# Performance work log

Measured on AMD Instinct MI355X. Metric: run time of the kernel, lower is better.

Reference implementation:

```python
import jax, jax.numpy as jnp
import numpy as np

BZ, NF, D = 8, 10000, 16
H = W = 512


def setup_inputs() -> dict:
    key = jax.random.key(0)
    k1, k2, k3 = jax.random.split(key, 3)
    attrs = jax.random.normal(k1, (BZ, NF, 3, D), dtype=jnp.float32)
    # barycentric weights: positive, sum to 1 over the 3 vertices
    u = jax.random.uniform(k2, (BZ, H, W, 3), dtype=jnp.float32, minval=1e-3, maxval=1.0)
    baryw_buffer = u / jnp.sum(u, axis=-1, keepdims=True)
    # triangle indices into the flattened [BZ*NF] face table; -1 = empty pixel
    triangle_buffer = jax.random.randint(k3, (BZ, H, W), -1, BZ * NF, dtype=jnp.int32)
    return {"attrs": attrs, "baryw_buffer": baryw_buffer, "triangle_buffer": triangle_buffer}


def reference(attrs, baryw_buffer, triangle_buffer):
    # attrs: [N, NF, 3, D]; baryw_buffer: [N, H, W, 3]; triangle_buffer: [N, H, W] int (-1 = bg)
    N, H_, W_ = triangle_buffer.shape
    Dd = attrs.shape[-1]
    flat_attrs = attrs.reshape(-1, 3, Dd)                      # [N*NF, 3, D]
    mask = triangle_buffer == -1                               # [N, H, W]
    idx = jnp.where(mask, 0, triangle_buffer)                  # clamp bg to 0
    pixel_face_vals = flat_attrs[idx]                          # [N, H, W, 3, D] gather
    pixel_vals = jnp.einsum('nhwk,nhwkd->nhwd', baryw_buffer, pixel_face_vals)
    pixel_vals = jnp.where(mask[..., None], 0.0, pixel_vals)   # zero background
    out = jnp.moveaxis(pixel_vals, -1, 1)                      # [N, D, H, W]
    vis = (~mask).astype(jnp.float32)[:, None]                 # [N, 1, H, W]
    return jnp.concatenate([out, vis], axis=1)                 # [N, D+1, H, W]
```

## Files before the change

### kernel.cpp

```cpp
#include <hip/hip_runtime.h>
#include <hip/hip_fp16.h>

constexpr int BZ = 8, NF = 10000, D = 16, HImg = 512, WImg = 512;
constexpr int HW = HImg * WImg;
constexpr int NPIX = BZ * HW;
constexpr int NFACES = BZ * NF;
constexpr int PIX_PER_THREAD = 4;
constexpr int NTHREADS = NPIX / PIX_PER_THREAD;
constexpr int BLOCK = 256;
constexpr size_t REC_USHORTS = 64;
constexpr size_t WS_NEEDED = (size_t)NFACES * 128;

__global__ __launch_bounds__(BLOCK) void convert_kernel(
    const float* __restrict__ attrs, ushort* __restrict__ rec)
{
    const int tid = blockIdx.x * BLOCK + threadIdx.x;
    if (tid >= NFACES * 6) return;
    const int face = tid / 6;
    const int c    = tid - face * 6;
    const float4* src = reinterpret_cast<const float4*>(
        attrs + (size_t)face * 48 + c * 8);
    const float4 a = src[0], b = src[1];
    __half h[8];
    h[0] = __float2half_rn(a.x); h[1] = __float2half_rn(a.y);
    h[2] = __float2half_rn(a.z); h[3] = __float2half_rn(a.w);
    h[4] = __float2half_rn(b.x); h[5] = __float2half_rn(b.y);
    h[6] = __float2half_rn(b.z); h[7] = __float2half_rn(b.w);
    *reinterpret_cast<int4*>(rec + (size_t)face * REC_USHORTS + c * 8) =
        *reinterpret_cast<const int4*>(h);
}

__device__ inline void h8_to_f8(int4 raw, float f[8]) {
    const __half2* hp = reinterpret_cast<const __half2*>(&raw);
#pragma unroll
    for (int q = 0; q < 4; ++q) {
        const float2 t = __half22float2(hp[q]);
        f[2 * q]     = t.x;
        f[2 * q + 1] = t.y;
    }
}

__global__ __launch_bounds__(BLOCK) void render_f16_kernel(
    const ushort* __restrict__ rec,
    const float*  __restrict__ baryw,
    const int*    __restrict__ tri,
    float*        __restrict__ out)
{
    const int tid = blockIdx.x * BLOCK + threadIdx.x;
    const int p0  = tid * PIX_PER_THREAD;
    if (p0 >= NPIX) return;

    const int n   = p0 / HW;
    const int pix = p0 - n * HW;

    const int4 t4 = *reinterpret_cast<const int4*>(tri + p0);
    const float4* bw = reinterpret_cast<const float4*>(baryw + (size_t)p0 * 3);
    const float4 b0 = bw[0], b1 = bw[1], b2 = bw[2];

    float w[PIX_PER_THREAD][3] = {
        {b0.x, b0.y, b0.z},
        {b0.w, b1.x, b1.y},
        {b1.z, b1.w, b2.x},
        {b2.y, b2.z, b2.w},
    };
    const int t[PIX_PER_THREAD] = {t4.x, t4.y, t4.z, t4.w};

    float vis[PIX_PER_THREAD];
    const int4* rbase[PIX_PER_THREAD];
#pragma unroll
    for (int j = 0; j < PIX_PER_THREAD; ++j) {
        const bool bg = (t[j] < 0);
        vis[j] = bg ? 0.0f : 1.0f;
        const int tc = bg ? 0 : t[j];
        rbase[j] = reinterpret_cast<const int4*>(rec) + (size_t)tc * 8;
        w[j][0] *= vis[j];
        w[j][1] *= vis[j];
        w[j][2] *= vis[j];
    }

    const size_t outbase = (size_t)n * (D + 1) * HW + pix;

#pragma unroll
    for (int c = 0; c < 2; ++c) {
        float r[PIX_PER_THREAD][8];
#pragma unroll
        for (int j = 0; j < PIX_PER_THREAD; ++j) {
            const int4 A0 = rbase[j][0 + c];
            const int4 A1 = rbase[j][2 + c];
            const int4 A2 = rbase[j][4 + c];
            float a0[8], a1[8], a2[8];
            h8_to_f8(A0, a0);
            h8_to_f8(A1, a1);
            h8_to_f8(A2, a2);
#pragma unroll
            for (int i = 0; i < 8; ++i)
                r[j][i] = w[j][0] * a0[i] + w[j][1] * a1[i] + w[j][2] * a2[i];
        }
#pragma unroll
        for (int i = 0; i < 8; ++i) {
            const int d = c * 8 + i;
            float4 o;
            o.x = r[0][i]; o.y = r[1][i]; o.z = r[2][i]; o.w = r[3][i];
            *reinterpret_cast<float4*>(out + outbase + (size_t)d * HW) = o;
        }
    }

    float4 v;
    v.x = vis[0]; v.y = vis[1]; v.z = vis[2]; v.w = vis[3];
    *reinterpret_cast<float4*>(out + outbase + (size_t)D * HW) = v;
}

__global__ __launch_bounds__(BLOCK) void renderer_f32_kernel(
    const float* __restrict__ attrs,
    const float* __restrict__ baryw,
    const int*   __restrict__ tri,
    float*       __restrict__ out)
{
    const int tid = blockIdx.x * BLOCK + threadIdx.x;
    const int p0  = tid * PIX_PER_THREAD;
    if (p0 >= NPIX) return;

    const int n   = p0 / HW;
    const int pix = p0 - n * HW;

    const int4 t4 = *reinterpret_cast<const int4*>(tri + p0);
    const float4* bw = reinterpret_cast<const float4*>(baryw + (size_t)p0 * 3);
    const float4 b0 = bw[0], b1 = bw[1], b2 = bw[2];

    float w[PIX_PER_THREAD][3] = {
        {b0.x, b0.y, b0.z},
        {b0.w, b1.x, b1.y},
        {b1.z, b1.w, b2.x},
        {b2.y, b2.z, b2.w},
    };
    const int t[PIX_PER_THREAD] = {t4.x, t4.y, t4.z, t4.w};

    float vis[PIX_PER_THREAD];
    const float4* abase[PIX_PER_THREAD];
#pragma unroll
    for (int j = 0; j < PIX_PER_THREAD; ++j) {
        const bool bg = (t[j] < 0);
        vis[j] = bg ? 0.0f : 1.0f;
        const int tc = bg ? 0 : t[j];
        abase[j] = reinterpret_cast<const float4*>(attrs + (size_t)tc * (3 * D));
        w[j][0] *= vis[j];
        w[j][1] *= vis[j];
        w[j][2] *= vis[j];
    }

    const size_t outbase = (size_t)n * (D + 1) * HW + pix;

#pragma unroll
    for (int c = 0; c < 4; ++c) {
        float r[PIX_PER_THREAD][4];
#pragma unroll
        for (int j = 0; j < PIX_PER_THREAD; ++j) {
            const float4 a0 = abase[j][c];
            const float4 a1 = abase[j][4 + c];
            const float4 a2 = abase[j][8 + c];
            r[j][0] = w[j][0] * a0.x + w[j][1] * a1.x + w[j][2] * a2.x;
            r[j][1] = w[j][0] * a0.y + w[j][1] * a1.y + w[j][2] * a2.y;
            r[j][2] = w[j][0] * a0.z + w[j][1] * a1.z + w[j][2] * a2.z;
            r[j][3] = w[j][0] * a0.w + w[j][1] * a1.w + w[j][2] * a2.w;
        }
#pragma unroll
        for (int i = 0; i < 4; ++i) {
            const int d = c * 4 + i;
            float4 o;
            o.x = r[0][i]; o.y = r[1][i]; o.z = r[2][i]; o.w = r[3][i];
            *reinterpret_cast<float4*>(out + outbase + (size_t)d * HW) = o;
        }
    }

    float4 v;
    v.x = vis[0]; v.y = vis[1]; v.z = vis[2]; v.w = vis[3];
    *reinterpret_cast<float4*>(out + outbase + (size_t)D * HW) = v;
}

extern "C" void kernel_launch(void* const* d_in, const int* in_sizes, int n_in,
                              void* d_out, int out_size, void* d_ws, size_t ws_size,
                              hipStream_t stream) {
    const float* attrs = (const float*)d_in[0];
    const float* baryw = (const float*)d_in[1];
    const int*   tri   = (const int*)d_in[2];
    float*       out   = (float*)d_out;

    const int grid = NTHREADS / BLOCK;

    if (ws_size >= WS_NEEDED) {
        ushort* rec = (ushort*)d_ws;
        const int conv_grid = (NFACES * 6 + BLOCK - 1) / BLOCK;
        convert_kernel<<<conv_grid, BLOCK, 0, stream>>>(attrs, rec);
        render_f16_kernel<<<grid, BLOCK, 0, stream>>>(rec, baryw, tri, out);
    } else {
        renderer_f32_kernel<<<grid, BLOCK, 0, stream>>>(attrs, baryw, tri, out);
    }
}
```

Before: 230.6 us.

## Phase face-record gathers by index range with block barriers and nontemporal streaming

The f16 render kernel now splits the face table into four index ranges and gathers, inside each range, only the pixels whose triangle falls there. Block-level barriers between phases try to keep the gather working set small enough to stay cache-resident. Streaming inputs and outputs use nontemporal loads and stores so they do not evict the face records. The cost is extra barriers and divergent, predicated gathers. Block-level syncs do not align phases across the whole GPU, so the locality benefit is uncertain.

```diff
diff --git a/kernel.cpp b/kernel.cpp
--- a/kernel.cpp
+++ b/kernel.cpp
@@ -10,6 +10,12 @@
 constexpr int BLOCK = 256;
 constexpr size_t REC_USHORTS = 64;
 constexpr size_t WS_NEEDED = (size_t)NFACES * 128;
+
+constexpr int NPHASE = 4;
+constexpr int FACES_PER_PHASE = NFACES / NPHASE;
+
+typedef float f32x4 __attribute__((ext_vector_type(4)));
+typedef int   i32x4 __attribute__((ext_vector_type(4)));
 
 __global__ __launch_bounds__(BLOCK) void convert_kernel(
     const float* __restrict__ attrs, ushort* __restrict__ rec)
@@ -40,7 +46,7 @@
     }
 }
 
-__global__ __launch_bounds__(BLOCK) void render_f16_kernel(
+__global__ __launch_bounds__(BLOCK) void render_f16_phased_kernel(
     const ushort* __restrict__ rec,
     const float*  __restrict__ baryw,
     const int*    __restrict__ tri,
@@ -48,14 +54,16 @@
 {
     const int tid = blockIdx.x * BLOCK + threadIdx.x;
     const int p0  = tid * PIX_PER_THREAD;
-    if (p0 >= NPIX) return;
 
     const int n   = p0 / HW;
     const int pix = p0 - n * HW;
 
-    const int4 t4 = *reinterpret_cast<const int4*>(tri + p0);
-    const float4* bw = reinterpret_cast<const float4*>(baryw + (size_t)p0 * 3);
-    const float4 b0 = bw[0], b1 = bw[1], b2 = bw[2];
+    const i32x4 t4 = __builtin_nontemporal_load(
+        reinterpret_cast<const i32x4*>(tri + p0));
+    const f32x4* bw = reinterpret_cast<const f32x4*>(baryw + (size_t)p0 * 3);
+    const f32x4 b0 = __builtin_nontemporal_load(bw + 0);
+    const f32x4 b1 = __builtin_nontemporal_load(bw + 1);
+    const f32x4 b2 = __builtin_nontemporal_load(bw + 2);
 
     float w[PIX_PER_THREAD][3] = {
         {b0.x, b0.y, b0.z},
@@ -66,48 +74,64 @@
     const int t[PIX_PER_THREAD] = {t4.x, t4.y, t4.z, t4.w};
 
     float vis[PIX_PER_THREAD];
-    const int4* rbase[PIX_PER_THREAD];
 #pragma unroll
     for (int j = 0; j < PIX_PER_THREAD; ++j) {
         const bool bg = (t[j] < 0);
         vis[j] = bg ? 0.0f : 1.0f;
-        const int tc = bg ? 0 : t[j];
-        rbase[j] = reinterpret_cast<const int4*>(rec) + (size_t)tc * 8;
         w[j][0] *= vis[j];
         w[j][1] *= vis[j];
         w[j][2] *= vis[j];
     }
 
     const size_t outbase = (size_t)n * (D + 1) * HW + pix;
+    const int4* rec4 = reinterpret_cast<const int4*>(rec);
 
 #pragma unroll
     for (int c = 0; c < 2; ++c) {
         float r[PIX_PER_THREAD][8];
 #pragma unroll
-        for (int j = 0; j < PIX_PER_THREAD; ++j) {
-            const int4 A0 = rbase[j][0 + c];
-            const int4 A1 = rbase[j][2 + c];
-            const int4 A2 = rbase[j][4 + c];
-            float a0[8], a1[8], a2[8];
-            h8_to_f8(A0, a0);
-            h8_to_f8(A1, a1);
-            h8_to_f8(A2, a2);
-#pragma unroll
-            for (int i = 0; i < 8; ++i)
-                r[j][i] = w[j][0] * a0[i] + w[j][1] * a1[i] + w[j][2] * a2[i];
-        }
+        for (int j = 0; j < PIX_PER_THREAD; ++j)
+#pragma unroll
+            for (int i = 0; i < 8; ++i) r[j][i] = 0.0f;
+
+#pragma unroll
+        for (int ph = 0; ph < NPHASE; ++ph) {
+            const int lo = ph * FACES_PER_PHASE;
+#pragma unroll
+            for (int j = 0; j < PIX_PER_THREAD; ++j) {
+                if ((unsigned)(t[j] - lo) < (unsigned)FACES_PER_PHASE) {
+                    const int4* rb = rec4 + (size_t)t[j] * 8;
+                    const int4 A0 = rb[0 + c];
+                    const int4 A1 = rb[2 + c];
+                    const int4 A2 = rb[4 + c];
+                    float a0[8], a1[8], a2[8];
+                    h8_to_f8(A0, a0);
+                    h8_to_f8(A1, a1);
+                    h8_to_f8(A2, a2);
+#pragma unroll
+                    for (int i = 0; i < 8; ++i)
+                        r[j][i] += w[j][0] * a0[i] + w[j][1] * a1[i]
+                                 + w[j][2] * a2[i];
+                }
+            }
+            if (ph != NPHASE - 1) __syncthreads();
+        }
+
 #pragma unroll
         for (int i = 0; i < 8; ++i) {
             const int d = c * 8 + i;
-            float4 o;
+            f32x4 o;
             o.x = r[0][i]; o.y = r[1][i]; o.z = r[2][i]; o.w = r[3][i];
-            *reinterpret_cast<float4*>(out + outbase + (size_t)d * HW) = o;
-        }
-    }
-
-    float4 v;
+            __builtin_nontemporal_store(
+                o, reinterpret_cast<f32x4*>(out + outbase + (size_t)d * HW));
+        }
+        if (c == 0) __syncthreads();
+    }
+
+    f32x4 v;
     v.x = vis[0]; v.y = vis[1]; v.z = vis[2]; v.w = vis[3];
-    *reinterpret_cast<float4*>(out + outbase + (size_t)D * HW) = v;
+    __builtin_nontemporal_store(
+        v, reinterpret_cast<f32x4*>(out + outbase + (size_t)D * HW));
 }
 
 __global__ __launch_bounds__(BLOCK) void renderer_f32_kernel(
@@ -191,7 +215,7 @@
         ushort* rec = (ushort*)d_ws;
         const int conv_grid = (NFACES * 6 + BLOCK - 1) / BLOCK;
         convert_kernel<<<conv_grid, BLOCK, 0, stream>>>(attrs, rec);
-        render_f16_kernel<<<grid, BLOCK, 0, stream>>>(rec, baryw, tri, out);
+        render_f16_phased_kernel<<<grid, BLOCK, 0, stream>>>(rec, baryw, tri, out);
     } else {
         renderer_f32_kernel<<<grid, BLOCK, 0, stream>>>(attrs, baryw, tri, out);
     }
```

Result: faster. 217.5 us (-5.7%).
